# Kernel optimization log

Hardware: AMD Instinct MI355X
Metric: run time of the kernel (lower is better)

## Reference

```python
import jax, jax.numpy as jnp
import numpy as np

B, T, C, H = 4, 2048, 1024, 16
D = C // H  # head_dim = 64


def setup_inputs() -> dict:
    key = jax.random.key(0)
    k1, k2, k3, k4, k5 = jax.random.split(key, 5)
    x = jax.random.normal(k1, (B, T, C), jnp.float32)
    w_qkv = jax.random.normal(k2, (3 * C, C), jnp.float32) * 0.02
    w_proj = jax.random.normal(k3, (C, C), jnp.float32) * 0.02
    b_proj = jax.random.normal(k4, (C,), jnp.float32) * 0.02
    # torch.randperm(T): a fixed random permutation of the keys
    perm = jax.random.permutation(k5, T).astype(jnp.int32)
    return {"x": x, "w_qkv": w_qkv, "w_proj": w_proj, "b_proj": b_proj, "perm": perm}


def reference(x, w_qkv, w_proj, b_proj, perm):
    Bx, Tx, Cx = x.shape
    # QKV projection (no bias), split into heads: (B, H, T, D)
    qkv = (x @ w_qkv.T).reshape(Bx, Tx, 3, H, D)
    q, k, v = jnp.moveaxis(qkv, 2, 0)            # each (B, T, H, D)
    q = q.transpose(0, 2, 1, 3)                   # (B, H, T, D)
    k = k.transpose(0, 2, 1, 3)
    v = v.transpose(0, 2, 1, 3)
    scale = 1.0 / np.float32(np.sqrt(D))
    scores = jnp.einsum('bhqd,bhkd->bhqk', q, k) * scale  # (B, H, T, T)
    # permuted causal mask: query i may attend to key j iff perm[j] <= i
    allowed = perm[None, :] <= jnp.arange(Tx)[:, None]     # (T, T) bool
    scores = jnp.where(allowed[None, None], scores, -jnp.inf)
    att = jax.nn.softmax(scores, axis=-1)
    y = jnp.einsum('bhqk,bhkd->bhqd', att, v)              # (B, H, T, D)
    y = y.transpose(0, 2, 1, 3).reshape(Bx, Tx, Cx)        # (B, T, C)
    return y @ w_proj.T + b_proj
```

## Files before the change

kernel.cpp:

```cpp
#include <hip/hip_runtime.h>
#include <stdint.h>

#define T_   2048
#define NH   16
#define HD   64
#define NBH  64
#define CDIM 1024
#define MROWS 8192

typedef __attribute__((ext_vector_type(8))) short short8;
typedef __attribute__((ext_vector_type(4))) float f32x4;
typedef __attribute__((ext_vector_type(16))) float f32x16;
typedef __attribute__((ext_vector_type(2))) unsigned int uint32x2;

#define LOG2E 1.44269504088896340736f

static __device__ __forceinline__ uint16_t f2bf(float f) {
  uint32_t u = __float_as_uint(f);
  return (uint16_t)((u + 0x7FFFu + ((u >> 16) & 1u)) >> 16);
}

static __device__ __forceinline__ void async16(const void* g, void* l) {
  __builtin_amdgcn_global_load_lds(
      (const __attribute__((address_space(1))) uint32_t*)g,
      (__attribute__((address_space(3))) uint32_t*)l, 16, 0, 0);
}

static __device__ __forceinline__ uint32x2 plswap(uint32_t a, uint32_t b) {
  return __builtin_amdgcn_permlane32_swap(a, b, false, false);
}
static __device__ __forceinline__ float halves_max(float x) {
  uint32x2 r = plswap(__float_as_uint(x), __float_as_uint(x));
  return fmaxf(__uint_as_float(r[0]), __uint_as_float(r[1]));
}
static __device__ __forceinline__ float halves_sum(float x) {
  uint32x2 r = plswap(__float_as_uint(x), __float_as_uint(x));
  return __uint_as_float(r[0]) + __uint_as_float(r[1]);
}
static __device__ __forceinline__ uint32_t pkbf(float lo, float hi) {
  uint32_t r;
  asm("v_cvt_pk_bf16_f32 %0, %1, %2" : "=v"(r) : "v"(lo), "v"(hi));
  return r;
}
static __device__ __forceinline__ float tmax32(const f32x16& a, const f32x16& b) {
  float t[16];
#pragma unroll
  for (int r = 0; r < 16; ++r) t[r] = fmaxf(a[r], b[r]);
#pragma unroll
  for (int s = 8; s >= 1; s >>= 1)
#pragma unroll
    for (int r = 0; r < s; ++r) t[r] = fmaxf(t[r], t[r + s]);
  return t[0];
}
static __device__ __forceinline__ float tsum32(const f32x16& a, const f32x16& b) {
  float t[16];
#pragma unroll
  for (int r = 0; r < 16; ++r) t[r] = a[r] + b[r];
#pragma unroll
  for (int s = 8; s >= 1; s >>= 1)
#pragma unroll
    for (int r = 0; r < s; ++r) t[r] += t[r + s];
  return t[0];
}

__global__ __launch_bounds__(256) void cvt3_f32_bf16(
    const float* __restrict__ a, uint16_t* __restrict__ oa, int na,
    const float* __restrict__ b, uint16_t* __restrict__ ob, int nb,
    const float* __restrict__ c, uint16_t* __restrict__ oc, int nc) {
  const int stride = gridDim.x * 256 * 4;
  for (int i = (blockIdx.x * 256 + threadIdx.x) * 4; i < na; i += stride) {
    float4 v = *(const float4*)(a + i);
    ushort4 o; o.x = f2bf(v.x); o.y = f2bf(v.y); o.z = f2bf(v.z); o.w = f2bf(v.w);
    *(ushort4*)(oa + i) = o;
  }
  for (int i = (blockIdx.x * 256 + threadIdx.x) * 4; i < nb; i += stride) {
    float4 v = *(const float4*)(b + i);
    ushort4 o; o.x = f2bf(v.x); o.y = f2bf(v.y); o.z = f2bf(v.z); o.w = f2bf(v.w);
    *(ushort4*)(ob + i) = o;
  }
  for (int i = (blockIdx.x * 256 + threadIdx.x) * 4; i < nc; i += stride) {
    float4 v = *(const float4*)(c + i);
    ushort4 o; o.x = f2bf(v.x); o.y = f2bf(v.y); o.z = f2bf(v.z); o.w = f2bf(v.w);
    *(ushort4*)(oc + i) = o;
  }
}

template <int MODE>
__global__ __launch_bounds__(256) void gemm_bt(
    const uint16_t* __restrict__ A, const uint16_t* __restrict__ Bt,
    float* __restrict__ Cout, const float* __restrict__ bias,
    uint16_t* __restrict__ Qo, uint16_t* __restrict__ Ko, uint16_t* __restrict__ Vo,
    const int* __restrict__ perm, int N) {
  __shared__ __attribute__((aligned(16))) uint16_t lds[8192];
  uint16_t* lA = lds;
  uint16_t* lB = lds + 4096;

  const int t = threadIdx.x;
  const int lane = t & 63, wv = t >> 6;
  const int gq = lane >> 4, lc = lane & 15;
  const int mbase = blockIdx.x * 128;
  const int nbase = blockIdx.y * 128;
  const int wr = (wv >> 1) * 64, wc = (wv & 1) * 64;

  f32x4 acc[4][4];
#pragma unroll
  for (int i = 0; i < 4; ++i)
#pragma unroll
    for (int j = 0; j < 4; ++j) acc[i][j] = (f32x4){0.f, 0.f, 0.f, 0.f};

  const int srow = t >> 2;
  const int scb  = (((t & 3) ^ ((t >> 3) & 3)) * 16);
  const int rxs  = (lc >> 1) & 3;

  for (int kt = 0; kt < 32; ++kt) {
    const char* baseA = (const char*)A + ((size_t)mbase * CDIM + kt * 32) * 2;
    const char* baseB = (const char*)Bt + ((size_t)nbase * CDIM + kt * 32) * 2;
#pragma unroll
    for (int j = 0; j < 2; ++j) {
      int row = j * 64 + srow;
      async16(baseA + (size_t)row * (CDIM * 2) + scb, (char*)lA + j * 4096 + wv * 1024);
    }
#pragma unroll
    for (int j = 0; j < 2; ++j) {
      int row = j * 64 + srow;
      async16(baseB + (size_t)row * (CDIM * 2) + scb, (char*)lB + j * 4096 + wv * 1024);
    }
    asm volatile("s_waitcnt vmcnt(0)" ::: "memory");
    __syncthreads();

    short8 af[4], bfr[4];
#pragma unroll
    for (int mi = 0; mi < 4; ++mi)
      af[mi] = *(const short8*)&lA[(wr + mi * 16 + lc) * 32 + ((gq ^ rxs) * 8)];
#pragma unroll
    for (int ni = 0; ni < 4; ++ni)
      bfr[ni] = *(const short8*)&lB[(wc + ni * 16 + lc) * 32 + ((gq ^ rxs) * 8)];
#pragma unroll
    for (int mi = 0; mi < 4; ++mi)
#pragma unroll
      for (int ni = 0; ni < 4; ++ni)
        acc[mi][ni] = __builtin_amdgcn_mfma_f32_16x16x32_bf16(af[mi], bfr[ni], acc[mi][ni], 0, 0, 0);
    __syncthreads();
  }

  if (MODE == 0) {
#pragma unroll
    for (int mi = 0; mi < 4; ++mi) {
      int row = mbase + wr + mi * 16 + 4 * gq;
#pragma unroll
      for (int ni = 0; ni < 4; ++ni) {
        int col = nbase + wc + ni * 16 + lc;
        float bv = bias[col];
#pragma unroll
        for (int r = 0; r < 4; ++r)
          Cout[(size_t)(row + r) * N + col] = acc[mi][ni][r] + bv;
      }
    }
  } else {
    const int wcw = wv & 1;
    for (int pass = 0; pass < 2; ++pass) {
#pragma unroll
      for (int mi = 0; mi < 4; ++mi) {
#pragma unroll
        for (int nj = 0; nj < 2; ++nj) {
          int ni = 2 * pass + nj;
          int colg = nbase + wc + ni * 16 + lc;
          bool isQ = (colg < 1024);
          int c64 = wcw * 32 + nj * 16 + lc;
          int within = c64 & 7;
#pragma unroll
          for (int r = 0; r < 4; ++r) {
            int row = wr + mi * 16 + 4 * gq + r;
            int swz = ((row >> 2) & 3) << 1;
            int ch = (c64 >> 3) ^ swz;
            float v = acc[mi][ni][r];
            if (isQ) v *= (0.125f * LOG2E);
            lds[row * 64 + ch * 8 + within] = f2bf(v);
          }
        }
      }
      __syncthreads();
#pragma unroll
      for (int k = 0; k < 4; ++k) {
        int v = 256 * k + t;
        int row = v >> 3;
        int ch = v & 7;
        int swz = ((row >> 2) & 3) << 1;
        short8 val = *(const short8*)&lds[row * 64 + ((ch ^ swz) * 8)];
        int m = mbase + row;
        int b = m >> 11, s = m & 2047;
        int p = perm[s];
        int colg = nbase + (ch >= 4 ? 64 : 0) + 32 * pass + (ch & 3) * 8;
        int typ = colg >> 10, cc = colg & 1023;
        int h = cc >> 6, d0 = cc & 63;
        int bh = b * 16 + h;
        if (typ == 0)
          *(short8*)(Qo + ((size_t)bh * T_ + s) * HD + d0) = val;
        else if (typ == 1)
          *(short8*)(Ko + ((size_t)bh * T_ + p) * HD + d0) = val;
        else
          *(short8*)(Vo + ((size_t)bh * T_ + p) * HD + d0) = val;
      }
      __syncthreads();
    }
  }
}

__global__ __launch_bounds__(256) void transpose_v(const uint16_t* __restrict__ Vp,
                                                   uint16_t* __restrict__ Vt) {
  __shared__ uint16_t tile[64][72];
  const int pb = blockIdx.x * 64;
  const int bh = blockIdx.y;
  const int t = threadIdx.x;
  const uint16_t* src = Vp + (size_t)bh * T_ * HD + (size_t)pb * HD;
#pragma unroll
  for (int it = 0; it < 2; ++it) {
    int lin = it * 256 + t;
    int row = lin >> 3, col = (lin & 7) * 8;
    short8 v = *(const short8*)(src + row * HD + col);
    *(short8*)&tile[row][col] = v;
  }
  __syncthreads();
  uint16_t* dst = Vt + (size_t)bh * HD * T_;
#pragma unroll
  for (int it = 0; it < 2; ++it) {
    int lin = it * 256 + t;
    int d = lin >> 3, ps = (lin & 7) * 8;
    short8 v;
#pragma unroll
    for (int j = 0; j < 8; ++j) v[j] = (short)tile[ps + j][d];
    *(short8*)(dst + (size_t)d * T_ + pb + ps) = v;
  }
}

__global__ __launch_bounds__(256, 4) void attn_kernel(
    const uint16_t* __restrict__ Q, const uint16_t* __restrict__ Kp,
    const uint16_t* __restrict__ Vt, uint16_t* __restrict__ Y) {
  __shared__ __attribute__((aligned(16))) uint16_t lK[2][64 * 64];
  __shared__ __attribute__((aligned(16))) uint16_t lV[2][64 * 64];

  const int bh = blockIdx.x;
  const int b = bh >> 4, h = bh & 15;
  const int pair = blockIdx.y;
  const int t = threadIdx.x;
  const int lane = t & 63, wv = t >> 6;
  const int l31 = lane & 31, hi = lane >> 5;

  const uint16_t* Kb = Kp + (size_t)bh * T_ * HD;
  const uint16_t* Vb = Vt + (size_t)bh * HD * T_;

  const int srow8 = lane >> 3;
  const int schunk = (lane & 7) ^ srow8;
  const int swz = (l31 & 7);

  for (int half = 0; half < 2; ++half) {
    const int qb = (half == 0 ? (15 - pair) : pair) * 128;
    const int qw = qb + 32 * wv;
    const int qg = qw + l31;

    const uint16_t* Qb = Q + ((size_t)bh * T_ + qw) * HD;

    short8 qf[4];
#pragma unroll
    for (int kc = 0; kc < 4; ++kc)
      qf[kc] = *(const short8*)(Qb + (size_t)l31 * HD + 16 * kc + 8 * hi);

    f32x16 ot[2];
#pragma unroll
    for (int dt = 0; dt < 2; ++dt)
#pragma unroll
      for (int r = 0; r < 16; ++r) ot[dt][r] = 0.f;
    float mrun = -__builtin_inff();
    float lrun = 0.f;

    const int nkt_blk = (qb >> 6) + 2;
    const int myKt = qw >> 6;

#pragma unroll
    for (int j = 0; j < 2; ++j) {
      int i = 2 * wv + j;
      async16(Kb + (size_t)(8 * i + srow8) * HD + schunk * 8,
              (char*)&lK[0][0] + i * 1024);
      async16(Vb + (size_t)(8 * i + srow8) * T_ + schunk * 8,
              (char*)&lV[0][0] + i * 1024);
    }

    for (int kt = 0; kt < nkt_blk; ++kt) {
      const int cur = kt & 1;
      const int p0 = kt * 64;
      if (kt + 1 < nkt_blk) {
        const int pn = p0 + 64;
#pragma unroll
        for (int j = 0; j < 2; ++j) {
          int i = 2 * wv + j;
          async16(Kb + (size_t)(pn + 8 * i + srow8) * HD + schunk * 8,
                  (char*)&lK[cur ^ 1][0] + i * 1024);
          async16(Vb + (size_t)(8 * i + srow8) * T_ + pn + schunk * 8,
                  (char*)&lV[cur ^ 1][0] + i * 1024);
        }
        asm volatile("s_waitcnt vmcnt(4)" ::: "memory");
      } else {
        asm volatile("s_waitcnt vmcnt(0)" ::: "memory");
      }
      __builtin_amdgcn_s_barrier();
      asm volatile("" ::: "memory");

      if (kt <= myKt) {
        const uint16_t* lk = &lK[cur][0];
        const uint16_t* lv = &lV[cur][0];

        f32x16 st[2];
#pragma unroll
        for (int a = 0; a < 2; ++a) {
          short8 kf[4];
#pragma unroll
          for (int kc = 0; kc < 4; ++kc)
            kf[kc] = *(const short8*)&lk[(32 * a + l31) * 64 + (((2 * kc + hi) ^ swz) * 8)];
#pragma unroll
          for (int r = 0; r < 16; ++r) st[a][r] = 0.f;
          __builtin_amdgcn_s_setprio(1);
#pragma unroll
          for (int kc = 0; kc < 4; ++kc)
            st[a] = __builtin_amdgcn_mfma_f32_32x32x16_bf16(kf[kc], qf[kc], st[a], 0, 0, 0);
          __builtin_amdgcn_s_setprio(0);
        }

        if (kt == myKt) {
#pragma unroll
          for (int a = 0; a < 2; ++a) {
            int kbase = p0 + 32 * a + 4 * hi;
#pragma unroll
            for (int r = 0; r < 16; ++r) {
              int key = kbase + (r & 3) + 8 * (r >> 2);
              if (key > qg) st[a][r] = -__builtin_inff();
            }
          }
        }

        float mall = halves_max(tmax32(st[0], st[1]));
        if (__any(mall > mrun + 8.0f)) {
          float mnew = fmaxf(mrun, mall);
          float alpha = __builtin_amdgcn_exp2f(mrun - mnew);
          mrun = mnew;
          lrun *= alpha;
#pragma unroll
          for (int dt = 0; dt < 2; ++dt)
#pragma unroll
            for (int r = 0; r < 16; ++r) ot[dt][r] *= alpha;
        }

#pragma unroll
        for (int a = 0; a < 2; ++a)
#pragma unroll
          for (int r = 0; r < 16; ++r)
            st[a][r] = __builtin_amdgcn_exp2f(st[a][r] - mrun);

        lrun += halves_sum(tsum32(st[0], st[1]));

        short8 pb[4];
#pragma unroll
        for (int kc = 0; kc < 4; ++kc) {
#define PV_(i) ((8 * kc + (i)) < 16 ? st[0][(8 * kc + (i)) & 15] : st[1][(8 * kc + (i)) & 15])
          uint32_t u0 = pkbf(PV_(0), PV_(1));
          uint32_t u1 = pkbf(PV_(2), PV_(3));
          uint32_t u2 = pkbf(PV_(4), PV_(5));
          uint32_t u3 = pkbf(PV_(6), PV_(7));
#undef PV_
          uint32x2 s02 = plswap(u0, u2);
          uint32x2 s13 = plswap(u1, u3);
          union { uint32_t w[4]; short8 s; } pbu;
          pbu.w[0] = s02[0]; pbu.w[1] = s13[0]; pbu.w[2] = s02[1]; pbu.w[3] = s13[1];
          pb[kc] = pbu.s;
        }

#pragma unroll
        for (int dt = 0; dt < 2; ++dt) {
          short8 vf[4];
#pragma unroll
          for (int kc = 0; kc < 4; ++kc)
            vf[kc] = *(const short8*)&lv[(32 * dt + l31) * 64 + (((2 * kc + hi) ^ swz) * 8)];
          __builtin_amdgcn_s_setprio(1);
#pragma unroll
          for (int kc = 0; kc < 4; ++kc)
            ot[dt] = __builtin_amdgcn_mfma_f32_32x32x16_bf16(vf[kc], pb[kc], ot[dt], 0, 0, 0);
          __builtin_amdgcn_s_setprio(0);
        }
      }
      asm volatile("" ::: "memory");
      __builtin_amdgcn_s_barrier();
    }

    float inv = 1.0f / lrun;
    uint16_t* Yrow = Y + ((size_t)b * T_ + qg) * CDIM + h * HD;
#pragma unroll
    for (int dt = 0; dt < 2; ++dt)
#pragma unroll
      for (int g = 0; g < 4; ++g) {
        int d0 = 32 * dt + 8 * g + 4 * hi;
        ushort4 o4;
        o4.x = f2bf(ot[dt][4 * g + 0] * inv);
        o4.y = f2bf(ot[dt][4 * g + 1] * inv);
        o4.z = f2bf(ot[dt][4 * g + 2] * inv);
        o4.w = f2bf(ot[dt][4 * g + 3] * inv);
        *(ushort4*)(Yrow + d0) = o4;
      }
  }
}

extern "C" void kernel_launch(void* const* d_in, const int* in_sizes, int n_in,
                              void* d_out, int out_size, void* d_ws, size_t ws_size,
                              hipStream_t stream) {
  const float* x = (const float*)d_in[0];
  const float* wqkv = (const float*)d_in[1];
  const float* wproj = (const float*)d_in[2];
  const float* bproj = (const float*)d_in[3];
  const int* perm = (const int*)d_in[4];
  float* out = (float*)d_out;

  char* ws = (char*)d_ws;
  uint16_t* xb     = (uint16_t*)(ws + 0);
  uint16_t* wqkvb  = (uint16_t*)(ws + 16777216);
  uint16_t* wprojb = (uint16_t*)(ws + 23068672);
  uint16_t* Qb     = (uint16_t*)(ws + 25165824);
  uint16_t* Kb     = (uint16_t*)(ws + 41943040);
  uint16_t* Vpb    = (uint16_t*)(ws + 58720256);
  uint16_t* Vtb    = (uint16_t*)(ws + 75497472);
  uint16_t* Yb     = xb;

  cvt3_f32_bf16<<<2048, 256, 0, stream>>>(x, xb, MROWS * CDIM,
                                          wqkv, wqkvb, 3 * CDIM * CDIM,
                                          wproj, wprojb, CDIM * CDIM);

  gemm_bt<1><<<dim3(64, 24), 256, 0, stream>>>(xb, wqkvb, nullptr, nullptr,
                                               Qb, Kb, Vpb, perm, 3072);
  transpose_v<<<dim3(32, 64), 256, 0, stream>>>(Vpb, Vtb);
  attn_kernel<<<dim3(64, 8), 256, 0, stream>>>(Qb, Kb, Vtb, Yb);
  gemm_bt<0><<<dim3(64, 8), 256, 0, stream>>>(Yb, wprojb, out, bproj,
                                              nullptr, nullptr, nullptr, nullptr, CDIM);
}
```

Before: 169.5 us.

## Process both query tiles of a pair concurrently in a 512-thread attention block

The attention block grows from 4 to 8 waves. The two paired query tiles (a late one and an early one) that were previously processed one after the other are now handled at the same time by two 4-wave groups, which share the K/V tiles staged in LDS. The stage loads are split so that waves 0-3 fetch K and waves 4-7 fetch V, and the blockIdx.y mapping changes to keep the pairing balanced. This halves each block's serial loop and reuses each K/V tile for both query tiles, at the cost of the short group idling at barriers while the long group runs and of higher per-block register and LDS pressure.

```diff
diff --git a/kernel.cpp b/kernel.cpp
--- a/kernel.cpp
+++ b/kernel.cpp
@@ -233,7 +233,7 @@
   }
 }
 
-__global__ __launch_bounds__(256, 4) void attn_kernel(
+__global__ __launch_bounds__(512, 4) void attn_kernel(
     const uint16_t* __restrict__ Q, const uint16_t* __restrict__ Kp,
     const uint16_t* __restrict__ Vt, uint16_t* __restrict__ Y) {
   __shared__ __attribute__((aligned(16))) uint16_t lK[2][64 * 64];
@@ -241,11 +241,20 @@
 
   const int bh = blockIdx.x;
   const int b = bh >> 4, h = bh & 15;
-  const int pair = blockIdx.y;
+  const int y = blockIdx.y;
+  const int pp = (y < 4) ? y : 11 - y;
   const int t = threadIdx.x;
   const int lane = t & 63, wv = t >> 6;
+  const int grp = wv >> 2;
+  const int wq = wv & 3;
   const int l31 = lane & 31, hi = lane >> 5;
 
+  const int qtile = grp == 0 ? (15 - pp) : pp;
+  const int qb = qtile * 128;
+  const int qw = qb + 32 * wq;
+  const int qg = qw + l31;
+
+  const uint16_t* Qb = Q + ((size_t)bh * T_ + qw) * HD;
   const uint16_t* Kb = Kp + (size_t)bh * T_ * HD;
   const uint16_t* Vb = Vt + (size_t)bh * HD * T_;
 
@@ -253,158 +262,150 @@
   const int schunk = (lane & 7) ^ srow8;
   const int swz = (l31 & 7);
 
-  for (int half = 0; half < 2; ++half) {
-    const int qb = (half == 0 ? (15 - pair) : pair) * 128;
-    const int qw = qb + 32 * wv;
-    const int qg = qw + l31;
-
-    const uint16_t* Qb = Q + ((size_t)bh * T_ + qw) * HD;
-
-    short8 qf[4];
-#pragma unroll
-    for (int kc = 0; kc < 4; ++kc)
-      qf[kc] = *(const short8*)(Qb + (size_t)l31 * HD + 16 * kc + 8 * hi);
-
-    f32x16 ot[2];
-#pragma unroll
-    for (int dt = 0; dt < 2; ++dt)
-#pragma unroll
-      for (int r = 0; r < 16; ++r) ot[dt][r] = 0.f;
-    float mrun = -__builtin_inff();
-    float lrun = 0.f;
-
-    const int nkt_blk = (qb >> 6) + 2;
-    const int myKt = qw >> 6;
-
-#pragma unroll
-    for (int j = 0; j < 2; ++j) {
-      int i = 2 * wv + j;
-      async16(Kb + (size_t)(8 * i + srow8) * HD + schunk * 8,
-              (char*)&lK[0][0] + i * 1024);
-      async16(Vb + (size_t)(8 * i + srow8) * T_ + schunk * 8,
-              (char*)&lV[0][0] + i * 1024);
-    }
-
-    for (int kt = 0; kt < nkt_blk; ++kt) {
-      const int cur = kt & 1;
-      const int p0 = kt * 64;
-      if (kt + 1 < nkt_blk) {
-        const int pn = p0 + 64;
-#pragma unroll
-        for (int j = 0; j < 2; ++j) {
-          int i = 2 * wv + j;
-          async16(Kb + (size_t)(pn + 8 * i + srow8) * HD + schunk * 8,
-                  (char*)&lK[cur ^ 1][0] + i * 1024);
-          async16(Vb + (size_t)(8 * i + srow8) * T_ + pn + schunk * 8,
-                  (char*)&lV[cur ^ 1][0] + i * 1024);
-        }
-        asm volatile("s_waitcnt vmcnt(4)" ::: "memory");
-      } else {
-        asm volatile("s_waitcnt vmcnt(0)" ::: "memory");
-      }
-      __builtin_amdgcn_s_barrier();
-      asm volatile("" ::: "memory");
-
-      if (kt <= myKt) {
-        const uint16_t* lk = &lK[cur][0];
-        const uint16_t* lv = &lV[cur][0];
-
-        f32x16 st[2];
+  short8 qf[4];
+#pragma unroll
+  for (int kc = 0; kc < 4; ++kc)
+    qf[kc] = *(const short8*)(Qb + (size_t)l31 * HD + 16 * kc + 8 * hi);
+
+  f32x16 ot[2];
+#pragma unroll
+  for (int dt = 0; dt < 2; ++dt)
+#pragma unroll
+    for (int r = 0; r < 16; ++r) ot[dt][r] = 0.f;
+  float mrun = -__builtin_inff();
+  float lrun = 0.f;
+
+  const int nkt_blk = 2 * (15 - pp) + 2;
+  const int myKt = qw >> 6;
+
+#define ASTAGE(pn, buf)                                                         \
+  {                                                                             \
+    _Pragma("unroll")                                                           \
+    for (int j = 0; j < 2; ++j) {                                               \
+      int i_ = 2 * wv + j;                                                      \
+      if (i_ < 8)                                                               \
+        async16(Kb + (size_t)((pn) + 8 * i_ + srow8) * HD + schunk * 8,         \
+                (char*)&lK[buf][0] + i_ * 1024);                                \
+      else                                                                      \
+        async16(Vb + (size_t)(8 * (i_ - 8) + srow8) * T_ + (pn) + schunk * 8,   \
+                (char*)&lV[buf][0] + (i_ - 8) * 1024);                          \
+    }                                                                           \
+  }
+
+  ASTAGE(0, 0);
+
+  for (int kt = 0; kt < nkt_blk; ++kt) {
+    const int cur = kt & 1;
+    const int p0 = kt * 64;
+    if (kt + 1 < nkt_blk) {
+      ASTAGE(p0 + 64, cur ^ 1);
+      asm volatile("s_waitcnt vmcnt(2)" ::: "memory");
+    } else {
+      asm volatile("s_waitcnt vmcnt(0)" ::: "memory");
+    }
+    __builtin_amdgcn_s_barrier();
+    asm volatile("" ::: "memory");
+
+    if (kt <= myKt) {
+      const uint16_t* lk = &lK[cur][0];
+      const uint16_t* lv = &lV[cur][0];
+
+      f32x16 st[2];
+#pragma unroll
+      for (int a = 0; a < 2; ++a) {
+        short8 kf[4];
+#pragma unroll
+        for (int kc = 0; kc < 4; ++kc)
+          kf[kc] = *(const short8*)&lk[(32 * a + l31) * 64 + (((2 * kc + hi) ^ swz) * 8)];
+#pragma unroll
+        for (int r = 0; r < 16; ++r) st[a][r] = 0.f;
+        __builtin_amdgcn_s_setprio(1);
+#pragma unroll
+        for (int kc = 0; kc < 4; ++kc)
+          st[a] = __builtin_amdgcn_mfma_f32_32x32x16_bf16(kf[kc], qf[kc], st[a], 0, 0, 0);
+        __builtin_amdgcn_s_setprio(0);
+      }
+
+      if (kt == myKt) {
 #pragma unroll
         for (int a = 0; a < 2; ++a) {
-          short8 kf[4];
-#pragma unroll
-          for (int kc = 0; kc < 4; ++kc)
-            kf[kc] = *(const short8*)&lk[(32 * a + l31) * 64 + (((2 * kc + hi) ^ swz) * 8)];
-#pragma unroll
-          for (int r = 0; r < 16; ++r) st[a][r] = 0.f;
-          __builtin_amdgcn_s_setprio(1);
-#pragma unroll
-          for (int kc = 0; kc < 4; ++kc)
-            st[a] = __builtin_amdgcn_mfma_f32_32x32x16_bf16(kf[kc], qf[kc], st[a], 0, 0, 0);
-          __builtin_amdgcn_s_setprio(0);
-        }
-
-        if (kt == myKt) {
-#pragma unroll
-          for (int a = 0; a < 2; ++a) {
-            int kbase = p0 + 32 * a + 4 * hi;
-#pragma unroll
-            for (int r = 0; r < 16; ++r) {
-              int key = kbase + (r & 3) + 8 * (r >> 2);
-              if (key > qg) st[a][r] = -__builtin_inff();
-            }
+          int kbase = p0 + 32 * a + 4 * hi;
+#pragma unroll
+          for (int r = 0; r < 16; ++r) {
+            int key = kbase + (r & 3) + 8 * (r >> 2);
+            if (key > qg) st[a][r] = -__builtin_inff();
           }
         }
-
-        float mall = halves_max(tmax32(st[0], st[1]));
-        if (__any(mall > mrun + 8.0f)) {
-          float mnew = fmaxf(mrun, mall);
-          float alpha = __builtin_amdgcn_exp2f(mrun - mnew);
-          mrun = mnew;
-          lrun *= alpha;
-#pragma unroll
-          for (int dt = 0; dt < 2; ++dt)
-#pragma unroll
-            for (int r = 0; r < 16; ++r) ot[dt][r] *= alpha;
-        }
-
-#pragma unroll
-        for (int a = 0; a < 2; ++a)
-#pragma unroll
-          for (int r = 0; r < 16; ++r)
-            st[a][r] = __builtin_amdgcn_exp2f(st[a][r] - mrun);
-
-        lrun += halves_sum(tsum32(st[0], st[1]));
-
-        short8 pb[4];
-#pragma unroll
-        for (int kc = 0; kc < 4; ++kc) {
+      }
+
+      float mall = halves_max(tmax32(st[0], st[1]));
+      if (__any(mall > mrun + 8.0f)) {
+        float mnew = fmaxf(mrun, mall);
+        float alpha = __builtin_amdgcn_exp2f(mrun - mnew);
+        mrun = mnew;
+        lrun *= alpha;
+#pragma unroll
+        for (int dt = 0; dt < 2; ++dt)
+#pragma unroll
+          for (int r = 0; r < 16; ++r) ot[dt][r] *= alpha;
+      }
+
+#pragma unroll
+      for (int a = 0; a < 2; ++a)
+#pragma unroll
+        for (int r = 0; r < 16; ++r)
+          st[a][r] = __builtin_amdgcn_exp2f(st[a][r] - mrun);
+
+      lrun += halves_sum(tsum32(st[0], st[1]));
+
+      short8 pb[4];
+#pragma unroll
+      for (int kc = 0; kc < 4; ++kc) {
 #define PV_(i) ((8 * kc + (i)) < 16 ? st[0][(8 * kc + (i)) & 15] : st[1][(8 * kc + (i)) & 15])
-          uint32_t u0 = pkbf(PV_(0), PV_(1));
-          uint32_t u1 = pkbf(PV_(2), PV_(3));
-          uint32_t u2 = pkbf(PV_(4), PV_(5));
-          uint32_t u3 = pkbf(PV_(6), PV_(7));
+        uint32_t u0 = pkbf(PV_(0), PV_(1));
+        uint32_t u1 = pkbf(PV_(2), PV_(3));
+        uint32_t u2 = pkbf(PV_(4), PV_(5));
+        uint32_t u3 = pkbf(PV_(6), PV_(7));
 #undef PV_
-          uint32x2 s02 = plswap(u0, u2);
-          uint32x2 s13 = plswap(u1, u3);
-          union { uint32_t w[4]; short8 s; } pbu;
-          pbu.w[0] = s02[0]; pbu.w[1] = s13[0]; pbu.w[2] = s02[1]; pbu.w[3] = s13[1];
-          pb[kc] = pbu.s;
-        }
-
-#pragma unroll
-        for (int dt = 0; dt < 2; ++dt) {
-          short8 vf[4];
-#pragma unroll
-          for (int kc = 0; kc < 4; ++kc)
-            vf[kc] = *(const short8*)&lv[(32 * dt + l31) * 64 + (((2 * kc + hi) ^ swz) * 8)];
-          __builtin_amdgcn_s_setprio(1);
-#pragma unroll
-          for (int kc = 0; kc < 4; ++kc)
-            ot[dt] = __builtin_amdgcn_mfma_f32_32x32x16_bf16(vf[kc], pb[kc], ot[dt], 0, 0, 0);
-          __builtin_amdgcn_s_setprio(0);
-        }
-      }
-      asm volatile("" ::: "memory");
-      __builtin_amdgcn_s_barrier();
-    }
-
-    float inv = 1.0f / lrun;
-    uint16_t* Yrow = Y + ((size_t)b * T_ + qg) * CDIM + h * HD;
-#pragma unroll
-    for (int dt = 0; dt < 2; ++dt)
-#pragma unroll
-      for (int g = 0; g < 4; ++g) {
-        int d0 = 32 * dt + 8 * g + 4 * hi;
-        ushort4 o4;
-        o4.x = f2bf(ot[dt][4 * g + 0] * inv);
-        o4.y = f2bf(ot[dt][4 * g + 1] * inv);
-        o4.z = f2bf(ot[dt][4 * g + 2] * inv);
-        o4.w = f2bf(ot[dt][4 * g + 3] * inv);
-        *(ushort4*)(Yrow + d0) = o4;
-      }
-  }
+        uint32x2 s02 = plswap(u0, u2);
+        uint32x2 s13 = plswap(u1, u3);
+        union { uint32_t w[4]; short8 s; } pbu;
+        pbu.w[0] = s02[0]; pbu.w[1] = s13[0]; pbu.w[2] = s02[1]; pbu.w[3] = s13[1];
+        pb[kc] = pbu.s;
+      }
+
+#pragma unroll
+      for (int dt = 0; dt < 2; ++dt) {
+        short8 vf[4];
+#pragma unroll
+        for (int kc = 0; kc < 4; ++kc)
+          vf[kc] = *(const short8*)&lv[(32 * dt + l31) * 64 + (((2 * kc + hi) ^ swz) * 8)];
+        __builtin_amdgcn_s_setprio(1);
+#pragma unroll
+        for (int kc = 0; kc < 4; ++kc)
+          ot[dt] = __builtin_amdgcn_mfma_f32_32x32x16_bf16(vf[kc], pb[kc], ot[dt], 0, 0, 0);
+        __builtin_amdgcn_s_setprio(0);
+      }
+    }
+    asm volatile("" ::: "memory");
+    __builtin_amdgcn_s_barrier();
+  }
+#undef ASTAGE
+
+  float inv = 1.0f / lrun;
+  uint16_t* Yrow = Y + ((size_t)b * T_ + qg) * CDIM + h * HD;
+#pragma unroll
+  for (int dt = 0; dt < 2; ++dt)
+#pragma unroll
+    for (int g = 0; g < 4; ++g) {
+      int d0 = 32 * dt + 8 * g + 4 * hi;
+      ushort4 o4;
+      o4.x = f2bf(ot[dt][4 * g + 0] * inv);
+      o4.y = f2bf(ot[dt][4 * g + 1] * inv);
+      o4.z = f2bf(ot[dt][4 * g + 2] * inv);
+      o4.w = f2bf(ot[dt][4 * g + 3] * inv);
+      *(ushort4*)(Yrow + d0) = o4;
+    }
 }
 
 extern "C" void kernel_launch(void* const* d_in, const int* in_sizes, int n_in,
@@ -434,7 +435,7 @@
   gemm_bt<1><<<dim3(64, 24), 256, 0, stream>>>(xb, wqkvb, nullptr, nullptr,
                                                Qb, Kb, Vpb, perm, 3072);
   transpose_v<<<dim3(32, 64), 256, 0, stream>>>(Vpb, Vtb);
-  attn_kernel<<<dim3(64, 8), 256, 0, stream>>>(Qb, Kb, Vtb, Yb);
+  attn_kernel<<<dim3(64, 8), 512, 0, stream>>>(Qb, Kb, Vtb, Yb);
   gemm_bt<0><<<dim3(64, 8), 256, 0, stream>>>(Yb, wprojb, out, bproj,
                                               nullptr, nullptr, nullptr, nullptr, CDIM);
 }
```

After: 164.5 us, median of 4. -2.9%, faster.
